# Kernel optimization log

Hardware: AMD Instinct MI355X
Metric: run time of the kernel (lower is better)

The kernel has to match this reference:

```python
import jax, jax.numpy as jnp
import numpy as np

B, S, IN_DIM, CTX = 32, 512, 256, 128
D, H, L = 128, 4, 2
DH = D // H
HID = 512
TOTAL = 11 * D * D + 8 * D  # hypernet flat weight size per sample
EPS = 1e-5


def _layernorm(x, g, b):
    mu = jnp.mean(x, axis=-1, keepdims=True)
    var = jnp.mean(jnp.square(x - mu), axis=-1, keepdims=True)
    return (x - mu) * jax.lax.rsqrt(var + EPS) * g + b


def setup_inputs() -> dict:
    key = jax.random.key(0)
    ks = jax.random.split(key, 24)
    f32 = jnp.float32
    inp = {
        'x': jax.random.normal(ks[0], (B, S, IN_DIM), f32),
        'context_vector': jax.random.normal(ks[1], (B, CTX), f32),
        'in_proj_w': jax.random.normal(ks[2], (D, IN_DIM), f32) * (IN_DIM ** -0.5),
        'in_proj_b': jnp.zeros((D,), f32),
        'pe': jax.random.normal(ks[3], (1, S, D), f32) * 0.02,
        'hfc1_w': jax.random.normal(ks[4], (L, HID, CTX), f32) * (CTX ** -0.5),
        'hfc1_b': jnp.zeros((L, HID), f32),
        'hfc2_w': jax.random.normal(ks[5], (L, TOTAL, HID), f32) * 0.02,
        'hfc2_b': jnp.zeros((L, TOTAL), f32),
        'out_proj_w': jax.random.normal(ks[6], (L, D, D), f32) * (D ** -0.5),
        'out_proj_b': jnp.zeros((L, D), f32),
        'ln1_g': jnp.ones((L, D), f32), 'ln1_b': jnp.zeros((L, D), f32),
        'ln2_g': jnp.ones((L, D), f32), 'ln2_b': jnp.zeros((L, D), f32),
        'alpha1': jnp.full((L,), 0.5, f32), 'alpha2': jnp.full((L,), 0.5, f32),
        'head_w': jax.random.normal(ks[7], (1, D), f32) * (D ** -0.5),
        'head_b': jnp.zeros((1,), f32),
    }
    return inp


def reference(x, context_vector, in_proj_w, in_proj_b, pe, hfc1_w, hfc1_b,
              hfc2_w, hfc2_b, out_proj_w, out_proj_b, ln1_g, ln1_b,
              ln2_g, ln2_b, alpha1, alpha2, head_w, head_b):
    # input projection + learned positional encoding
    h = jnp.einsum('bsi,di->bsd', x, in_proj_w) + in_proj_b
    h = h + pe[:, :h.shape[1], :]

    # flat split offsets for hypernet output
    sizes = [3 * D * D, 3 * D, 4 * D * D, 4 * D, 4 * D * D, D]
    offs = np.concatenate([[0], np.cumsum(sizes)])

    for l in range(L):
        # hypernet: per-sample weights from context
        hid = jax.nn.relu(context_vector @ hfc1_w[l].T + hfc1_b[l])
        flat = hid @ hfc2_w[l].T + hfc2_b[l]  # [B, TOTAL]
        aw = flat[:, offs[0]:offs[1]].reshape(B, 3 * D, D)
        ab = flat[:, offs[1]:offs[2]]                     # [B, 3D]
        f1w = flat[:, offs[2]:offs[3]].reshape(B, 4 * D, D)
        f1b = flat[:, offs[3]:offs[4]]                    # [B, 4D]
        f2w = flat[:, offs[4]:offs[5]].reshape(B, D, 4 * D)
        f2b = flat[:, offs[5]:offs[6]]                    # [B, D]

        # per-sample QKV projection (grouped GEMM over batch)
        qkv = jnp.einsum('bsd,bed->bse', h, aw) + ab[:, None, :]
        q, k, v = jnp.split(qkv, 3, axis=-1)
        q = q.reshape(B, S, H, DH)
        k = k.reshape(B, S, H, DH)
        v = v.reshape(B, S, H, DH)
        scores = jnp.einsum('bqhd,bkhd->bhqk', q, k) / jnp.sqrt(jnp.float32(DH))
        attn = jax.nn.softmax(scores, axis=-1)
        ctx = jnp.einsum('bhqk,bkhd->bqhd', attn, v).reshape(B, S, D)
        attn_out = jnp.einsum('bsd,ed->bse', ctx, out_proj_w[l]) + out_proj_b[l]

        h = _layernorm(h + alpha1[l] * attn_out, ln1_g[l], ln1_b[l])

        # per-sample FFN
        ff = jax.nn.relu(jnp.einsum('bsd,bfd->bsf', h, f1w) + f1b[:, None, :])
        ff = jnp.einsum('bsf,bdf->bsd', ff, f2w) + f2b[:, None, :]

        h = _layernorm(h + alpha2[l] * ff, ln2_g[l], ln2_b[l])

    out = h[:, -1, :] @ head_w.T + head_b  # [B, 1]
    return out
```

## Files before the change

### kernel.cpp

```cpp
#include <hip/hip_runtime.h>
#include <hip/hip_bf16.h>

constexpr int B_    = 32;
constexpr int S_    = 512;
constexpr int INDIM = 256;
constexpr int KCTX  = 128;
constexpr int D_    = 128;
constexpr int H_    = 4;
constexpr int L_    = 2;
constexpr int HID_  = 512;
constexpr int TOTAL_ = 11 * D_ * D_ + 8 * D_;
constexpr int OFF_AB  = 3 * D_ * D_;
constexpr int OFF_F1W = OFF_AB + 3 * D_;
constexpr int OFF_F1B = OFF_F1W + 4 * D_ * D_;
constexpr int OFF_F2W = OFF_F1B + 4 * D_;
constexpr int OFF_F2B = OFF_F2W + 4 * D_ * D_;
constexpr int TP = 132;

typedef __attribute__((ext_vector_type(8))) short short8;
typedef __attribute__((ext_vector_type(4))) short short4v;
typedef __attribute__((ext_vector_type(2))) short short2v;
typedef __attribute__((ext_vector_type(4))) float f32x4;

#define MFMA16 __builtin_amdgcn_mfma_f32_16x16x32_bf16

__device__ __forceinline__ short f2bf(float f) {
  __hip_bfloat16 h = __float2bfloat16(f);
  return __builtin_bit_cast(short, h);
}
__device__ __forceinline__ float bf2f(short s) {
  __hip_bfloat16 h = __builtin_bit_cast(__hip_bfloat16, s);
  return __bfloat162float(h);
}
struct bfpair { short hi, lo; };
__device__ __forceinline__ bfpair split2p(float x) {
  bfpair p;
  p.hi = f2bf(x);
  p.lo = f2bf(x - bf2f(p.hi));
  return p;
}

__device__ __forceinline__ void cvt_body(const float* __restrict__ in,
                                         short* __restrict__ oh,
                                         short* __restrict__ ol,
                                         int ktShift, int n8, int t) {
  if (t >= n8) return;
  int kt = 1 << ktShift;
  int row = t >> ktShift;
  int kc = t & (kt - 1);
  const float* p = in + ((long)row << (ktShift + 3)) + kc * 8;
  float4 v0 = *(const float4*)p;
  float4 v1 = *(const float4*)(p + 4);
  short8 h8, l8; bfpair q;
  q = split2p(v0.x); h8[0] = q.hi; l8[0] = q.lo;
  q = split2p(v0.y); h8[1] = q.hi; l8[1] = q.lo;
  q = split2p(v0.z); h8[2] = q.hi; l8[2] = q.lo;
  q = split2p(v0.w); h8[3] = q.hi; l8[3] = q.lo;
  q = split2p(v1.x); h8[4] = q.hi; l8[4] = q.lo;
  q = split2p(v1.y); h8[5] = q.hi; l8[5] = q.lo;
  q = split2p(v1.z); h8[6] = q.hi; l8[6] = q.lo;
  q = split2p(v1.w); h8[7] = q.hi; l8[7] = q.lo;
  long o = ((long)(row >> 4) * kt + kc) * 128 + (row & 15) * 8;
  *(short8*)(oh + o) = h8;
  *(short8*)(ol + o) = l8;
}

__global__ __launch_bounds__(256) void k_prep(
    const float* __restrict__ ipw, const float* __restrict__ opw,
    short* __restrict__ ipwFh, short* __restrict__ ipwFl,
    short* __restrict__ opwFh, short* __restrict__ opwFl,
    const float* __restrict__ cvec, const float* __restrict__ h1w,
    const float* __restrict__ h1b,
    short* __restrict__ hidFh, short* __restrict__ hidFl) {
  int id = blockIdx.x, tid = threadIdx.x;
  if (id < 16) {
    cvt_body(ipw, ipwFh, ipwFl, 5, D_ * INDIM / 8, id * 256 + tid);
  } else if (id < 32) {
    cvt_body(opw, opwFh, opwFl, 4, L_ * D_ * D_ / 8, (id - 16) * 256 + tid);
  } else {
    int hb = id - 32;
    int l = hb >> 5, b = hb & 31;
    __shared__ float cs[KCTX];
    if (tid < KCTX) cs[tid] = cvec[b * KCTX + tid];
    __syncthreads();
    #pragma unroll
    for (int jj = 0; jj < 2; ++jj) {
      int j = tid + jj * 256;
      const float* wr = h1w + (long)(l * HID_ + j) * KCTX;
      float s = h1b[l * HID_ + j];
      #pragma unroll
      for (int c = 0; c < KCTX; c += 4) {
        float4 cv = *(const float4*)(cs + c);
        float4 wv = *(const float4*)(wr + c);
        s += cv.x * wv.x + cv.y * wv.y + cv.z * wv.z + cv.w * wv.w;
      }
      s = fmaxf(s, 0.f);
      bfpair p = split2p(s);
      long o = (long)l * 32 * HID_ + ((long)(b >> 4) * 64 + (j >> 3)) * 128
             + (b & 15) * 8 + (j & 7);
      hidFh[o] = p.hi;
      hidFl[o] = p.lo;
    }
  }
}

__global__ __launch_bounds__(256) void k_flat_ip(
    const short* __restrict__ hidh, const short* __restrict__ hidl,
    const float* __restrict__ W, const float* __restrict__ bias,
    short* __restrict__ awh, short* __restrict__ awl,
    short* __restrict__ f1h, short* __restrict__ f1l,
    short* __restrict__ f2h, short* __restrict__ f2l,
    float* __restrict__ ab, float* __restrict__ f1b, float* __restrict__ f2b,
    const float* __restrict__ x,
    const short* __restrict__ ipwFh, const short* __restrict__ ipwFl,
    const float* __restrict__ ipb, const float* __restrict__ pe,
    float* __restrict__ h_f, short* __restrict__ hFh, short* __restrict__ hFl) {
  __shared__ short wls[2][2][64 * 64];
  const int id = blockIdx.x;
  const int tid = threadIdx.x, wave = tid >> 6, lane = tid & 63;
  const int r = lane & 15, g = lane >> 4;
  const int rr = tid >> 4;
  const int cc = (tid & 15) * 4;

  if (id < 256) {
    const int bx = id >> 5, b = id & 31;
    const float* abase = x + ((long)b * S_ + bx * 64) * INDIM;
    float4 av[2][4];
    #pragma unroll
    for (int rnd = 0; rnd < 4; ++rnd) {
      av[0][rnd] = *(const float4*)(abase + (long)(rnd * 16 + rr) * INDIM + cc);
      av[1][rnd] = *(const float4*)(abase + (long)(rnd * 16 + rr) * INDIM + 64 + cc);
    }
    const int n0 = (wave >> 1) * 64;
    const short* pWh = ipwFh + (n0 >> 4) * 4096 + g * 128 + r * 8;
    const short* pWl = ipwFl + (n0 >> 4) * 4096 + g * 128 + r * 8;
    f32x4 acc[2][4] = {{{0,0,0,0},{0,0,0,0},{0,0,0,0},{0,0,0,0}},
                       {{0,0,0,0},{0,0,0,0},{0,0,0,0},{0,0,0,0}}};
    for (int i = 0; i < 4; ++i) {
      int c0 = i * 64, cur = i & 1;
      #pragma unroll
      for (int rnd = 0; rnd < 4; ++rnd) {
        int row = rnd * 16 + rr;
        short4v h4, l4; bfpair q;
        q = split2p(av[cur][rnd].x); h4[0] = q.hi; l4[0] = q.lo;
        q = split2p(av[cur][rnd].y); h4[1] = q.hi; l4[1] = q.lo;
        q = split2p(av[cur][rnd].z); h4[2] = q.hi; l4[2] = q.lo;
        q = split2p(av[cur][rnd].w); h4[3] = q.hi; l4[3] = q.lo;
        int sb = row * 128 + ((cc * 2) ^ ((row & 7) << 4));
        *(short4v*)((char*)&wls[cur][0][0] + sb) = h4;
        *(short4v*)((char*)&wls[cur][1][0] + sb) = l4;
      }
      if (i + 2 < 4) {
        #pragma unroll
        for (int rnd = 0; rnd < 4; ++rnd)
          av[cur][rnd] = *(const float4*)(abase + (long)(rnd * 16 + rr) * INDIM + (c0 + 128) + cc);
      }
      __syncthreads();
      #pragma unroll
      for (int kk = 0; kk < 2; ++kk) {
        long wo = (long)(c0 * 16) + kk * 512;
        short8 ah[2], al[2];
        #pragma unroll
        for (int ms = 0; ms < 2; ++ms) {
          int arow = (wave & 1) * 32 + ms * 16 + r;
          int abyte = arow * 128 + ((kk * 64 + g * 16) ^ ((r & 7) << 4));
          ah[ms] = *(const short8*)((char*)&wls[cur][0][0] + abyte);
          al[ms] = *(const short8*)((char*)&wls[cur][1][0] + abyte);
        }
        #pragma unroll
        for (int ns = 0; ns < 4; ++ns) {
          short8 wh = *(const short8*)(pWh + ns * 4096 + wo);
          short8 wl = *(const short8*)(pWl + ns * 4096 + wo);
          #pragma unroll
          for (int ms = 0; ms < 2; ++ms) {
            acc[ms][ns] = MFMA16(ah[ms], wl, acc[ms][ns], 0, 0, 0);
            acc[ms][ns] = MFMA16(al[ms], wh, acc[ms][ns], 0, 0, 0);
            acc[ms][ns] = MFMA16(ah[ms], wh, acc[ms][ns], 0, 0, 0);
          }
        }
      }
      __syncthreads();
    }
    #pragma unroll
    for (int ms = 0; ms < 2; ++ms) {
      #pragma unroll
      for (int ns = 0; ns < 4; ++ns) {
        int ccol = n0 + ns * 16 + r;
        float bv = ipb[ccol];
        #pragma unroll
        for (int reg = 0; reg < 4; ++reg) {
          int crow = bx * 64 + (wave & 1) * 32 + ms * 16 + g * 4 + reg;
          float v = acc[ms][ns][reg] + bv + pe[crow * D_ + ccol];
          h_f[((long)b * S_ + crow) * D_ + ccol] = v;
          long o = (long)b * 65536 + (long)(crow >> 4) * 2048
                 + (ccol >> 3) * 128 + (crow & 15) * 8 + (ccol & 7);
          bfpair sp = split2p(v);
          hFh[o] = sp.hi;
          hFl[o] = sp.lo;
        }
      }
    }
    return;
  }

  const int fid = id - 256;
  const int l = fid / 2832;
  const int bxf = fid % 2832;
  hidh += (long)l * 32 * HID_;
  hidl += (long)l * 32 * HID_;
  W    += (long)l * TOTAL_ * HID_;
  bias += (long)l * TOTAL_;
  awh  += (long)l * B_ * 49152;  awl += (long)l * B_ * 49152;
  f1h  += (long)l * B_ * 65536;  f1l += (long)l * B_ * 65536;
  f2h  += (long)l * B_ * 65536;  f2l += (long)l * B_ * 65536;
  ab   += l * B_ * 384;  f1b += l * B_ * 512;  f2b += l * B_ * 128;
  const int nb0 = bxf * 64;
  const float* wbase = W + (long)nb0 * HID_;
  float4 wv[2][4];
  #pragma unroll
  for (int rnd = 0; rnd < 4; ++rnd) {
    wv[0][rnd] = *(const float4*)(wbase + (long)(rnd * 16 + rr) * HID_ + cc);
    wv[1][rnd] = *(const float4*)(wbase + (long)(rnd * 16 + rr) * HID_ + 64 + cc);
  }
  const short* pAh = hidh + g * 128 + r * 8;
  const short* pAl = hidl + g * 128 + r * 8;
  f32x4 acc0 = {0, 0, 0, 0}, acc1 = {0, 0, 0, 0};
  for (int i = 0; i < 8; ++i) {
    int c0 = i * 64, cur = i & 1;
    #pragma unroll
    for (int rnd = 0; rnd < 4; ++rnd) {
      int row = rnd * 16 + rr;
      short4v h4, l4; bfpair q;
      q = split2p(wv[cur][rnd].x); h4[0] = q.hi; l4[0] = q.lo;
      q = split2p(wv[cur][rnd].y); h4[1] = q.hi; l4[1] = q.lo;
      q = split2p(wv[cur][rnd].z); h4[2] = q.hi; l4[2] = q.lo;
      q = split2p(wv[cur][rnd].w); h4[3] = q.hi; l4[3] = q.lo;
      int sb = row * 128 + ((cc * 2) ^ ((row & 7) << 4));
      *(short4v*)((char*)&wls[cur][0][0] + sb) = h4;
      *(short4v*)((char*)&wls[cur][1][0] + sb) = l4;
    }
    if (i + 2 < 8) {
      #pragma unroll
      for (int rnd = 0; rnd < 4; ++rnd)
        wv[cur][rnd] = *(const float4*)(wbase + (long)(rnd * 16 + rr) * HID_ + (c0 + 128) + cc);
    }
    __syncthreads();
    #pragma unroll
    for (int kk = 0; kk < 2; ++kk) {
      long ao = (long)(c0 * 16) + kk * 512;
      short8 ah0 = *(const short8*)(pAh + ao);
      short8 ah1 = *(const short8*)(pAh + 8192 + ao);
      short8 al0 = *(const short8*)(pAl + ao);
      short8 al1 = *(const short8*)(pAl + 8192 + ao);
      int wrow = wave * 16 + r;
      int wb = wrow * 128 + ((kk * 64 + g * 16) ^ ((r & 7) << 4));
      short8 wh = *(const short8*)((char*)&wls[cur][0][0] + wb);
      short8 wl = *(const short8*)((char*)&wls[cur][1][0] + wb);
      acc0 = MFMA16(ah0, wl, acc0, 0, 0, 0);
      acc0 = MFMA16(al0, wh, acc0, 0, 0, 0);
      acc0 = MFMA16(ah0, wh, acc0, 0, 0, 0);
      acc1 = MFMA16(ah1, wl, acc1, 0, 0, 0);
      acc1 = MFMA16(al1, wh, acc1, 0, 0, 0);
      acc1 = MFMA16(ah1, wh, acc1, 0, 0, 0);
    }
    __syncthreads();
  }
  constexpr int TPF = 68;
  float* tile = (float*)&wls[0][0][0];
  {
    float bv = bias[nb0 + wave * 16 + r];
    int col = wave * 16 + r;
    #pragma unroll
    for (int reg = 0; reg < 4; ++reg) {
      tile[(g * 4 + reg) * TPF + col]      = acc0[reg] + bv;
      tile[(g * 4 + reg + 16) * TPF + col] = acc1[reg] + bv;
    }
  }
  __syncthreads();
  {
    int b  = tid >> 3;
    int cg = tid & 7;
    int t0 = nb0 + cg * 8;
    float v[8];
    #pragma unroll
    for (int j = 0; j < 8; ++j) v[j] = tile[b * TPF + cg * 8 + j];
    if (t0 < OFF_AB) {
      int e = t0 >> 7, d = t0 & 127;
      long a = (long)b * 49152 + ((long)(e >> 4) * 16 + (d >> 3)) * 128 + (e & 15) * 8;
      short8 h8, l8; bfpair q;
      #pragma unroll
      for (int j = 0; j < 8; ++j) { q = split2p(v[j]); h8[j] = q.hi; l8[j] = q.lo; }
      *(short8*)(awh + a) = h8;
      *(short8*)(awl + a) = l8;
    } else if (t0 < OFF_F1W) {
      float* dst = ab + b * 384 + (t0 - OFF_AB);
      float4 x0 = {v[0], v[1], v[2], v[3]}, x1 = {v[4], v[5], v[6], v[7]};
      *(float4*)dst = x0; *(float4*)(dst + 4) = x1;
    } else if (t0 < OFF_F1B) {
      int i = t0 - OFF_F1W; int f = i >> 7, d = i & 127;
      long a = (long)b * 65536 + ((long)(f >> 4) * 16 + (d >> 3)) * 128 + (f & 15) * 8;
      short8 h8, l8; bfpair q;
      #pragma unroll
      for (int j = 0; j < 8; ++j) { q = split2p(v[j]); h8[j] = q.hi; l8[j] = q.lo; }
      *(short8*)(f1h + a) = h8;
      *(short8*)(f1l + a) = l8;
    } else if (t0 < OFF_F2W) {
      float* dst = f1b + b * 512 + (t0 - OFF_F1B);
      float4 x0 = {v[0], v[1], v[2], v[3]}, x1 = {v[4], v[5], v[6], v[7]};
      *(float4*)dst = x0; *(float4*)(dst + 4) = x1;
    } else if (t0 < OFF_F2B) {
      int i = t0 - OFF_F2W; int dd = i >> 9, f = i & 511;
      long a = (long)b * 65536 + ((long)(dd >> 4) * 64 + (f >> 3)) * 128 + (dd & 15) * 8;
      short8 h8, l8; bfpair q;
      #pragma unroll
      for (int j = 0; j < 8; ++j) { q = split2p(v[j]); h8[j] = q.hi; l8[j] = q.lo; }
      *(short8*)(f2h + a) = h8;
      *(short8*)(f2l + a) = l8;
    } else {
      float* dst = f2b + b * 128 + (t0 - OFF_F2B);
      float4 x0 = {v[0], v[1], v[2], v[3]}, x1 = {v[4], v[5], v[6], v[7]};
      *(float4*)dst = x0; *(float4*)(dst + 4) = x1;
    }
  }
}

template <int K, int EPI, bool RELU>
__global__ __launch_bounds__(256) void k_gemm(
    const short* __restrict__ Ah, const short* __restrict__ Al, long sA,
    const short* __restrict__ Wh, const short* __restrict__ Wl, long sW,
    const float* __restrict__ biasP, long sB,
    void* __restrict__ p0, void* __restrict__ p1,
    void* __restrict__ p2, void* __restrict__ p3,
    int N,
    const float* __restrict__ lng, const float* __restrict__ lnb,
    const float* __restrict__ lnal, int mOff, int nOff, int mode) {
  extern __shared__ char smem_dyn[];
  const int tid = threadIdx.x, wave = tid >> 6, lane = tid & 63;
  const int r = lane & 15, g = lane >> 4;
  const int b = blockIdx.z;
  int bx, by;
  if (mode == 1) {
    int xx = blockIdx.x;
    if (xx < 16) { bx = xx >> 1; by = 1 + (xx & 1); }
    else         { bx = 7; by = 0; }
  } else {
    bx = blockIdx.x + mOff; by = blockIdx.y + nOff;
  }
  const int m0 = bx * 64 + (wave & 1) * 32;
  const int n0 = by * 128 + (wave >> 1) * 64;
  const long KT = (long)K * 16;
  const short* pAh = Ah + (long)b * sA + (m0 >> 4) * KT + g * 128 + r * 8;
  const short* pAl = Al + (long)b * sA + (m0 >> 4) * KT + g * 128 + r * 8;
  const short* pWh = Wh + (long)b * sW + (n0 >> 4) * KT + g * 128 + r * 8;
  const short* pWl = Wl + (long)b * sW + (n0 >> 4) * KT + g * 128 + r * 8;
  f32x4 acc[2][4] = {{{0,0,0,0},{0,0,0,0},{0,0,0,0},{0,0,0,0}},
                     {{0,0,0,0},{0,0,0,0},{0,0,0,0},{0,0,0,0}}};
  for (int kk = 0; kk < K / 32; ++kk) {
    long ko = (long)kk * 512;
    short8 a0h = *(const short8*)(pAh + ko);
    short8 a1h = *(const short8*)(pAh + KT + ko);
    short8 a0l = *(const short8*)(pAl + ko);
    short8 a1l = *(const short8*)(pAl + KT + ko);
    #pragma unroll
    for (int ns = 0; ns < 4; ++ns) {
      short8 wh = *(const short8*)(pWh + ns * KT + ko);
      short8 wl = *(const short8*)(pWl + ns * KT + ko);
      acc[0][ns] = MFMA16(a0h, wl, acc[0][ns], 0, 0, 0);
      acc[0][ns] = MFMA16(a0l, wh, acc[0][ns], 0, 0, 0);
      acc[0][ns] = MFMA16(a0h, wh, acc[0][ns], 0, 0, 0);
      acc[1][ns] = MFMA16(a1h, wl, acc[1][ns], 0, 0, 0);
      acc[1][ns] = MFMA16(a1l, wh, acc[1][ns], 0, 0, 0);
      acc[1][ns] = MFMA16(a1h, wh, acc[1][ns], 0, 0, 0);
    }
  }

  if constexpr (EPI == 5) {
    if (by == 2) {
      #pragma unroll
      for (int ms = 0; ms < 2; ++ms) {
        int crow0 = m0 + ms * 16 + g * 4;
        #pragma unroll
        for (int ns = 0; ns < 4; ++ns) {
          int ccol = n0 + ns * 16 + r;
          float bv = biasP[(long)b * sB + ccol];
          int c2 = ccol - 256, hd = c2 >> 5, dd = c2 & 31;
          short4v h4, l4; bfpair q;
          #pragma unroll
          for (int reg = 0; reg < 4; ++reg) {
            float v = acc[ms][ns][reg] + bv;
            q = split2p(v); h4[reg] = q.hi; l4[reg] = q.lo;
          }
          long o = (long)(b * 4 + hd) * 16384 + (dd >> 4) * 8192
                 + (crow0 >> 3) * 128 + (dd & 15) * 8 + (crow0 & 7);
          *(short4v*)((short*)p2 + o) = h4;
          *(short4v*)((short*)p3 + o) = l4;
        }
      }
      return;
    }
  }

  float* tile = (float*)smem_dyn;
  #pragma unroll
  for (int ms = 0; ms < 2; ++ms) {
    #pragma unroll
    for (int ns = 0; ns < 4; ++ns) {
      int ccol = n0 + ns * 16 + r;
      float bv = biasP[(long)b * sB + ccol];
      #pragma unroll
      for (int reg = 0; reg < 4; ++reg) {
        float v = acc[ms][ns][reg] + bv;
        if constexpr (RELU) v = fmaxf(v, 0.f);
        int trow2 = (wave & 1) * 32 + ms * 16 + g * 4 + reg;
        int tcol = (wave >> 1) * 64 + ns * 16 + r;
        tile[trow2 * TP + tcol] = v;
      }
    }
  }
  __syncthreads();

  if constexpr (EPI == 0 || EPI == 5) {
    int row = tid >> 2, cg = tid & 3;
    int crow = bx * 64 + row;
    long rowbase = (long)b * 512 * N + (long)(crow >> 4) * (16 * (long)N) + (crow & 15) * 8;
    #pragma unroll
    for (int j4 = 0; j4 < 4; ++j4) {
      int tcol = j4 * 32 + cg * 8;
      float4 aa = *(const float4*)&tile[row * TP + tcol];
      float4 bb = *(const float4*)&tile[row * TP + tcol + 4];
// ... 157 lines not shown
      int col0 = hh * 32 + r;
      long o = (long)b * 65536 + (long)(srow >> 4) * 2048
             + (col0 >> 3) * 128 + (srow & 15) * 8 + (col0 & 7);
      bfpair sp0 = split2p(a0);
      ch[o] = sp0.hi; cl[o] = sp0.lo;
      long o2 = o + 2 * 128;
      bfpair sp1 = split2p(a1);
      ch[o2] = sp1.hi; cl[o2] = sp1.lo;
    }
  }
}

__global__ __launch_bounds__(64) void k_head(const float* __restrict__ h,
                                             const float* __restrict__ hw,
                                             const float* __restrict__ hb,
                                             float* __restrict__ out) {
  int b = blockIdx.x, lane = threadIdx.x;
  const float* hr = h + ((long)b * S_ + (S_ - 1)) * D_;
  float v = hr[lane] * hw[lane] + hr[lane + 64] * hw[lane + 64];
  #pragma unroll
  for (int o = 32; o > 0; o >>= 1) v += __shfl_xor(v, o);
  if (lane == 0) out[b] = v + hb[0];
}

extern "C" void kernel_launch(void* const* d_in, const int* in_sizes, int n_in,
                              void* d_out, int out_size, void* d_ws, size_t ws_size,
                              hipStream_t stream) {
  const float* x    = (const float*)d_in[0];
  const float* cvec = (const float*)d_in[1];
  const float* ipw  = (const float*)d_in[2];
  const float* ipb  = (const float*)d_in[3];
  const float* pe   = (const float*)d_in[4];
  const float* h1w  = (const float*)d_in[5];
  const float* h1b  = (const float*)d_in[6];
  const float* h2w  = (const float*)d_in[7];
  const float* h2b  = (const float*)d_in[8];
  const float* opw  = (const float*)d_in[9];
  const float* opb  = (const float*)d_in[10];
  const float* ln1g = (const float*)d_in[11];
  const float* ln1b = (const float*)d_in[12];
  const float* ln2g = (const float*)d_in[13];
  const float* ln2b = (const float*)d_in[14];
  const float* a1   = (const float*)d_in[15];
  const float* a2   = (const float*)d_in[16];
  const float* hw   = (const float*)d_in[17];
  const float* hb   = (const float*)d_in[18];
  float* out = (float*)d_out;

  char* ws = (char*)d_ws;
  size_t off = 0;
  auto alloc = [&](size_t n) { void* p = ws + off; off = (off + n + 255) & ~(size_t)255; return p; };

  const long AWs = (long)B_ * 49152;
  const long F1s = (long)B_ * 65536;
  const long F2s = (long)B_ * 65536;

  short* ff1h  = (short*)alloc((size_t)B_ * S_ * 512 * 2);
  short* ff1l  = (short*)alloc((size_t)B_ * S_ * 512 * 2);
  float* h_f   = (float*)alloc((size_t)B_ * S_ * D_ * 4);
  short* hFh   = (short*)alloc((size_t)B_ * S_ * D_ * 2);
  short* hFl   = (short*)alloc((size_t)B_ * S_ * D_ * 2);
  short* hidFh = (short*)alloc((size_t)L_ * 32 * HID_ * 2);
  short* hidFl = (short*)alloc((size_t)L_ * 32 * HID_ * 2);
  short* awFh  = (short*)alloc((size_t)L_ * AWs * 2);
  short* awFl  = (short*)alloc((size_t)L_ * AWs * 2);
  short* f1wFh = (short*)alloc((size_t)L_ * F1s * 2);
  short* f1wFl = (short*)alloc((size_t)L_ * F1s * 2);
  short* f2wFh = (short*)alloc((size_t)L_ * F2s * 2);
  short* f2wFl = (short*)alloc((size_t)L_ * F2s * 2);
  float* abF   = (float*)alloc((size_t)L_ * B_ * 384 * 4);
  float* f1bF  = (float*)alloc((size_t)L_ * B_ * 512 * 4);
  float* f2bF  = (float*)alloc((size_t)L_ * B_ * 128 * 4);
  short* qkFh  = (short*)alloc((size_t)B_ * S_ * 256 * 2);
  short* qkFl  = (short*)alloc((size_t)B_ * S_ * 256 * 2);
  short* vtFh  = (short*)alloc((size_t)B_ * H_ * 32 * S_ * 2);
  short* vtFl  = (short*)alloc((size_t)B_ * H_ * 32 * S_ * 2);
  short* cxFh  = (short*)alloc((size_t)B_ * S_ * D_ * 2);
  short* cxFl  = (short*)alloc((size_t)B_ * S_ * D_ * 2);
  short* ipwFh = (short*)alloc((size_t)D_ * INDIM * 2);
  short* ipwFl = (short*)alloc((size_t)D_ * INDIM * 2);
  short* opwFh = (short*)alloc((size_t)L_ * D_ * D_ * 2);
  short* opwFl = (short*)alloc((size_t)L_ * D_ * D_ * 2);

  k_prep<<<96, 256, 0, stream>>>(ipw, opw, ipwFh, ipwFl, opwFh, opwFl,
                                 cvec, h1w, h1b, hidFh, hidFl);

  k_flat_ip<<<256 + 2 * 2832, 256, 0, stream>>>(
      hidFh, hidFl, h2w, h2b, awFh, awFl, f1wFh, f1wFl, f2wFh, f2wFl,
      abF, f1bF, f2bF,
      x, ipwFh, ipwFl, ipb, pe, h_f, hFh, hFl);

  constexpr size_t TILE_LDS = 64 * TP * 4;

  {
    int l = 0;
    k_gemm<D_, 5, false><<<dim3(8, 3, B_), 256, TILE_LDS, stream>>>(
        hFh, hFl, (long)S_ * D_, awFh + l * AWs, awFl + l * AWs, 49152,
        abF + l * B_ * 384, 384,
        qkFh, qkFl, vtFh, vtFl, 256, nullptr, nullptr, nullptr, 0, 0, 0);
    k_attn<<<dim3(S_ / 16, H_, B_), 128, 0, stream>>>(qkFh, qkFl, vtFh, vtFl, cxFh, cxFl, 0);
    k_gemm<D_, 4, false><<<dim3(8, 1, B_), 256, TILE_LDS, stream>>>(
        cxFh, cxFl, (long)S_ * D_, opwFh + l * 16384, opwFl + l * 16384, 0,
        opb + l * D_, 0, h_f, hFh, hFl, nullptr, 128,
        ln1g + l * D_, ln1b + l * D_, a1 + l, 0, 0, 0);
    k_gemm<D_, 0, true><<<dim3(8, 4, B_), 256, TILE_LDS, stream>>>(
        hFh, hFl, (long)S_ * D_, f1wFh + l * F1s, f1wFl + l * F1s, 65536,
        f1bF + l * B_ * 512, 512,
        ff1h, ff1l, nullptr, nullptr, 512, nullptr, nullptr, nullptr, 0, 0, 0);
    k_gemm<512, 4, false><<<dim3(8, 1, B_), 256, TILE_LDS, stream>>>(
        ff1h, ff1l, (long)S_ * 512, f2wFh + l * F2s, f2wFl + l * F2s, 65536,
        f2bF + l * B_ * 128, 128,
        h_f, hFh, hFl, nullptr, 128,
        ln2g + l * D_, ln2b + l * D_, a2 + l, 0, 0, 0);
  }

  {
    int l = 1;
    k_gemm<D_, 5, false><<<dim3(17, 1, B_), 256, TILE_LDS, stream>>>(
        hFh, hFl, (long)S_ * D_, awFh + l * AWs, awFl + l * AWs, 49152,
        abF + l * B_ * 384, 384,
        qkFh, qkFl, vtFh, vtFl, 256, nullptr, nullptr, nullptr, 0, 0, 1);
    k_attn<<<dim3(1, H_, B_), 128, 0, stream>>>(qkFh, qkFl, vtFh, vtFl, cxFh, cxFl, 31);
    k_gemm<D_, 4, false><<<dim3(1, 1, B_), 256, TILE_LDS, stream>>>(
        cxFh, cxFl, (long)S_ * D_, opwFh + l * 16384, opwFl + l * 16384, 0,
        opb + l * D_, 0, h_f, hFh, hFl, nullptr, 128,
        ln1g + l * D_, ln1b + l * D_, a1 + l, 7, 0, 0);
    k_gemm<D_, 0, true><<<dim3(1, 4, B_), 256, TILE_LDS, stream>>>(
        hFh, hFl, (long)S_ * D_, f1wFh + l * F1s, f1wFl + l * F1s, 65536,
        f1bF + l * B_ * 512, 512,
        ff1h, ff1l, nullptr, nullptr, 512, nullptr, nullptr, nullptr, 7, 0, 0);
    k_gemm<512, 4, false><<<dim3(1, 1, B_), 256, TILE_LDS, stream>>>(
        ff1h, ff1l, (long)S_ * 512, f2wFh + l * F2s, f2wFl + l * F2s, 65536,
        f2bF + l * B_ * 128, 128,
        h_f, hFh, hFl, nullptr, 128,
        ln2g + l * D_, ln2b + l * D_, a2 + l, 7, 0, 0);
  }
  k_head<<<B_, 64, 0, stream>>>(h_f, hw, hb, out);
}
```

Before: 417.1 us.

## Overlap layer-1 hypernet weight generation with layer-0 GEMM kernels

Moves the layer-1 hypernet flat-weight GEMM out of the initial k_flat_ip launch and spreads its 2832 blocks across the four layer-0 k_gemm launches as extra trailing blocks. The GEMM kernels switch to a 1D grid with a gemmBlocks threshold, and blocks past it run flat_block using the dynamic LDS. The aim is to fill idle CUs during the small per-layer GEMMs and shorten the large upfront hypernet kernel. In exchange, the layer-0 kernels carry more register and LDS pressure from the merged code path, and the dynamic LDS must be large enough for flat_block's buffers.

```diff
diff --git a/kernel.cpp b/kernel.cpp
--- a/kernel.cpp
+++ b/kernel.cpp
@@ -104,6 +104,217 @@
   }
 }
 
+__device__ void flat_block(int fid, char* lds,
+    const short* __restrict__ hidh, const short* __restrict__ hidl,
+    const float* __restrict__ W, const float* __restrict__ bias,
+    short* __restrict__ awh, short* __restrict__ awl,
+    short* __restrict__ f1h, short* __restrict__ f1l,
+    short* __restrict__ f2h, short* __restrict__ f2l,
+    float* __restrict__ ab, float* __restrict__ f1b, float* __restrict__ f2b) {
+  const int tid = threadIdx.x, wave = tid >> 6, lane = tid & 63;
+  const int r = lane & 15, g = lane >> 4;
+  const int rr = tid >> 4, cc = (tid & 15) * 4;
+  const int nb0 = fid * 64;
+  const float* wbase = W + (long)nb0 * HID_;
+  float4 wv[2][4];
+  #pragma unroll
+  for (int rnd = 0; rnd < 4; ++rnd) {
+    wv[0][rnd] = *(const float4*)(wbase + (long)(rnd * 16 + rr) * HID_ + cc);
+    wv[1][rnd] = *(const float4*)(wbase + (long)(rnd * 16 + rr) * HID_ + 64 + cc);
+  }
+  const short* pAh = hidh + g * 128 + r * 8;
+  const short* pAl = hidl + g * 128 + r * 8;
+  f32x4 acc0 = {0, 0, 0, 0}, acc1 = {0, 0, 0, 0};
+  for (int i = 0; i < 8; ++i) {
+    int c0 = i * 64, cur = i & 1;
+    char* bh = lds + (cur * 2 + 0) * 8192;
+    char* bl = lds + (cur * 2 + 1) * 8192;
+    #pragma unroll
+    for (int rnd = 0; rnd < 4; ++rnd) {
+      int row = rnd * 16 + rr;
+      short4v h4, l4; bfpair q;
+      q = split2p(wv[cur][rnd].x); h4[0] = q.hi; l4[0] = q.lo;
+      q = split2p(wv[cur][rnd].y); h4[1] = q.hi; l4[1] = q.lo;
+      q = split2p(wv[cur][rnd].z); h4[2] = q.hi; l4[2] = q.lo;
+      q = split2p(wv[cur][rnd].w); h4[3] = q.hi; l4[3] = q.lo;
+      int sb = row * 128 + ((cc * 2) ^ ((row & 7) << 4));
+      *(short4v*)(bh + sb) = h4;
+      *(short4v*)(bl + sb) = l4;
+    }
+    if (i + 2 < 8) {
+      #pragma unroll
+      for (int rnd = 0; rnd < 4; ++rnd)
+        wv[cur][rnd] = *(const float4*)(wbase + (long)(rnd * 16 + rr) * HID_ + (c0 + 128) + cc);
+    }
+    __syncthreads();
+    #pragma unroll
+    for (int kk = 0; kk < 2; ++kk) {
+      long ao = (long)(c0 * 16) + kk * 512;
+      short8 ah0 = *(const short8*)(pAh + ao);
+      short8 ah1 = *(const short8*)(pAh + 8192 + ao);
+      short8 al0 = *(const short8*)(pAl + ao);
+      short8 al1 = *(const short8*)(pAl + 8192 + ao);
+      int wrow = wave * 16 + r;
+      int wb = wrow * 128 + ((kk * 64 + g * 16) ^ ((r & 7) << 4));
+      short8 wh = *(const short8*)(bh + wb);
+      short8 wl = *(const short8*)(bl + wb);
+      acc0 = MFMA16(ah0, wl, acc0, 0, 0, 0);
+      acc0 = MFMA16(al0, wh, acc0, 0, 0, 0);
+      acc0 = MFMA16(ah0, wh, acc0, 0, 0, 0);
+      acc1 = MFMA16(ah1, wl, acc1, 0, 0, 0);
+      acc1 = MFMA16(al1, wh, acc1, 0, 0, 0);
+      acc1 = MFMA16(ah1, wh, acc1, 0, 0, 0);
+    }
+    __syncthreads();
+  }
+  constexpr int TPF = 68;
+  float* tile = (float*)lds;
+  {
+    float bv = bias[nb0 + wave * 16 + r];
+    int col = wave * 16 + r;
+    #pragma unroll
+    for (int reg = 0; reg < 4; ++reg) {
+      tile[(g * 4 + reg) * TPF + col]      = acc0[reg] + bv;
+      tile[(g * 4 + reg + 16) * TPF + col] = acc1[reg] + bv;
+    }
+  }
+  __syncthreads();
+  {
+    int b  = tid >> 3;
+    int cg = tid & 7;
+    int t0 = nb0 + cg * 8;
+    float v[8];
+    #pragma unroll
+    for (int j = 0; j < 8; ++j) v[j] = tile[b * TPF + cg * 8 + j];
+    if (t0 < OFF_AB) {
+      int e = t0 >> 7, d = t0 & 127;
+      long a = (long)b * 49152 + ((long)(e >> 4) * 16 + (d >> 3)) * 128 + (e & 15) * 8;
+      short8 h8, l8; bfpair q;
+      #pragma unroll
+      for (int j = 0; j < 8; ++j) { q = split2p(v[j]); h8[j] = q.hi; l8[j] = q.lo; }
+      *(short8*)(awh + a) = h8;
+      *(short8*)(awl + a) = l8;
+    } else if (t0 < OFF_F1W) {
+      float* dst = ab + b * 384 + (t0 - OFF_AB);
+      float4 x0 = {v[0], v[1], v[2], v[3]}, x1 = {v[4], v[5], v[6], v[7]};
+      *(float4*)dst = x0; *(float4*)(dst + 4) = x1;
+    } else if (t0 < OFF_F1B) {
+      int i = t0 - OFF_F1W; int f = i >> 7, d = i & 127;
+      long a = (long)b * 65536 + ((long)(f >> 4) * 16 + (d >> 3)) * 128 + (f & 15) * 8;
+      short8 h8, l8; bfpair q;
+      #pragma unroll
+      for (int j = 0; j < 8; ++j) { q = split2p(v[j]); h8[j] = q.hi; l8[j] = q.lo; }
+      *(short8*)(f1h + a) = h8;
+      *(short8*)(f1l + a) = l8;
+    } else if (t0 < OFF_F2W) {
+      float* dst = f1b + b * 512 + (t0 - OFF_F1B);
+      float4 x0 = {v[0], v[1], v[2], v[3]}, x1 = {v[4], v[5], v[6], v[7]};
+      *(float4*)dst = x0; *(float4*)(dst + 4) = x1;
+    } else if (t0 < OFF_F2B) {
+      int i = t0 - OFF_F2W; int dd = i >> 9, f = i & 511;
+      long a = (long)b * 65536 + ((long)(dd >> 4) * 64 + (f >> 3)) * 128 + (dd & 15) * 8;
+      short8 h8, l8; bfpair q;
+      #pragma unroll
+      for (int j = 0; j < 8; ++j) { q = split2p(v[j]); h8[j] = q.hi; l8[j] = q.lo; }
+      *(short8*)(f2h + a) = h8;
+      *(short8*)(f2l + a) = l8;
+    } else {
+      float* dst = f2b + b * 128 + (t0 - OFF_F2B);
+      float4 x0 = {v[0], v[1], v[2], v[3]}, x1 = {v[4], v[5], v[6], v[7]};
+      *(float4*)dst = x0; *(float4*)(dst + 4) = x1;
+    }
+  }
+}
+
+__device__ void inproj_block(int id, char* lds,
+    const float* __restrict__ x,
+    const short* __restrict__ ipwFh, const short* __restrict__ ipwFl,
+    const float* __restrict__ ipb, const float* __restrict__ pe,
+    float* __restrict__ h_f, short* __restrict__ hFh, short* __restrict__ hFl) {
+  const int tid = threadIdx.x, wave = tid >> 6, lane = tid & 63;
+  const int r = lane & 15, g = lane >> 4;
+  const int rr = tid >> 4, cc = (tid & 15) * 4;
+  const int bx = id >> 5, b = id & 31;
+  const float* abase = x + ((long)b * S_ + bx * 64) * INDIM;
+  float4 av[2][4];
+  #pragma unroll
+  for (int rnd = 0; rnd < 4; ++rnd) {
+    av[0][rnd] = *(const float4*)(abase + (long)(rnd * 16 + rr) * INDIM + cc);
+    av[1][rnd] = *(const float4*)(abase + (long)(rnd * 16 + rr) * INDIM + 64 + cc);
+  }
+  const int n0 = (wave >> 1) * 64;
+  const short* pWh = ipwFh + (n0 >> 4) * 4096 + g * 128 + r * 8;
+  const short* pWl = ipwFl + (n0 >> 4) * 4096 + g * 128 + r * 8;
+  f32x4 acc[2][4] = {{{0,0,0,0},{0,0,0,0},{0,0,0,0},{0,0,0,0}},
+                     {{0,0,0,0},{0,0,0,0},{0,0,0,0},{0,0,0,0}}};
+  for (int i = 0; i < 4; ++i) {
+    int c0 = i * 64, cur = i & 1;
+    char* bh = lds + (cur * 2 + 0) * 8192;
+    char* bl = lds + (cur * 2 + 1) * 8192;
+    #pragma unroll
+    for (int rnd = 0; rnd < 4; ++rnd) {
+      int row = rnd * 16 + rr;
+      short4v h4, l4; bfpair q;
+      q = split2p(av[cur][rnd].x); h4[0] = q.hi; l4[0] = q.lo;
+      q = split2p(av[cur][rnd].y); h4[1] = q.hi; l4[1] = q.lo;
+      q = split2p(av[cur][rnd].z); h4[2] = q.hi; l4[2] = q.lo;
+      q = split2p(av[cur][rnd].w); h4[3] = q.hi; l4[3] = q.lo;
+      int sb = row * 128 + ((cc * 2) ^ ((row & 7) << 4));
+      *(short4v*)(bh + sb) = h4;
+      *(short4v*)(bl + sb) = l4;
+    }
+    if (i + 2 < 4) {
+      #pragma unroll
+      for (int rnd = 0; rnd < 4; ++rnd)
+        av[cur][rnd] = *(const float4*)(abase + (long)(rnd * 16 + rr) * INDIM + (c0 + 128) + cc);
+    }
+    __syncthreads();
+    #pragma unroll
+    for (int kk = 0; kk < 2; ++kk) {
+      long wo = (long)(c0 * 16) + kk * 512;
+      short8 ah[2], al[2];
+      #pragma unroll
+      for (int ms = 0; ms < 2; ++ms) {
+        int arow = (wave & 1) * 32 + ms * 16 + r;
+        int abyte = arow * 128 + ((kk * 64 + g * 16) ^ ((r & 7) << 4));
+        ah[ms] = *(const short8*)(bh + abyte);
+        al[ms] = *(const short8*)(bl + abyte);
+      }
+      #pragma unroll
+      for (int ns = 0; ns < 4; ++ns) {
+        short8 wh = *(const short8*)(pWh + ns * 4096 + wo);
+        short8 wl = *(const short8*)(pWl + ns * 4096 + wo);
+        #pragma unroll
+        for (int ms = 0; ms < 2; ++ms) {
+          acc[ms][ns] = MFMA16(ah[ms], wl, acc[ms][ns], 0, 0, 0);
+          acc[ms][ns] = MFMA16(al[ms], wh, acc[ms][ns], 0, 0, 0);
+          acc[ms][ns] = MFMA16(ah[ms], wh, acc[ms][ns], 0, 0, 0);
+        }
+      }
+    }
+    __syncthreads();
+  }
+  #pragma unroll
+  for (int ms = 0; ms < 2; ++ms) {
+    #pragma unroll
+    for (int ns = 0; ns < 4; ++ns) {
+      int ccol = n0 + ns * 16 + r;
+      float bv = ipb[ccol];
+      #pragma unroll
+      for (int reg = 0; reg < 4; ++reg) {
+        int crow = bx * 64 + (wave & 1) * 32 + ms * 16 + g * 4 + reg;
+        float v = acc[ms][ns][reg] + bv + pe[crow * D_ + ccol];
+        h_f[((long)b * S_ + crow) * D_ + ccol] = v;
+        long o = (long)b * 65536 + (long)(crow >> 4) * 2048
+               + (ccol >> 3) * 128 + (crow & 15) * 8 + (ccol & 7);
+        bfpair sp = split2p(v);
+        hFh[o] = sp.hi;
+        hFl[o] = sp.lo;
+      }
+    }
+  }
+}
+
 __global__ __launch_bounds__(256) void k_flat_ip(
     const short* __restrict__ hidh, const short* __restrict__ hidl,
     const float* __restrict__ W, const float* __restrict__ bias,
@@ -115,212 +326,13 @@
     const short* __restrict__ ipwFh, const short* __restrict__ ipwFl,
     const float* __restrict__ ipb, const float* __restrict__ pe,
     float* __restrict__ h_f, short* __restrict__ hFh, short* __restrict__ hFl) {
-  __shared__ short wls[2][2][64 * 64];
+  __shared__ __align__(16) char ldsb[33792];
   const int id = blockIdx.x;
-  const int tid = threadIdx.x, wave = tid >> 6, lane = tid & 63;
-  const int r = lane & 15, g = lane >> 4;
-  const int rr = tid >> 4;
-  const int cc = (tid & 15) * 4;
-
   if (id < 256) {
-    const int bx = id >> 5, b = id & 31;
-    const float* abase = x + ((long)b * S_ + bx * 64) * INDIM;
-    float4 av[2][4];
-    #pragma unroll
-    for (int rnd = 0; rnd < 4; ++rnd) {
-      av[0][rnd] = *(const float4*)(abase + (long)(rnd * 16 + rr) * INDIM + cc);
-      av[1][rnd] = *(const float4*)(abase + (long)(rnd * 16 + rr) * INDIM + 64 + cc);
-    }
-    const int n0 = (wave >> 1) * 64;
-    const short* pWh = ipwFh + (n0 >> 4) * 4096 + g * 128 + r * 8;
-    const short* pWl = ipwFl + (n0 >> 4) * 4096 + g * 128 + r * 8;
-    f32x4 acc[2][4] = {{{0,0,0,0},{0,0,0,0},{0,0,0,0},{0,0,0,0}},
-                       {{0,0,0,0},{0,0,0,0},{0,0,0,0},{0,0,0,0}}};
-    for (int i = 0; i < 4; ++i) {
-      int c0 = i * 64, cur = i & 1;
-      #pragma unroll
-      for (int rnd = 0; rnd < 4; ++rnd) {
-        int row = rnd * 16 + rr;
-        short4v h4, l4; bfpair q;
-        q = split2p(av[cur][rnd].x); h4[0] = q.hi; l4[0] = q.lo;
-        q = split2p(av[cur][rnd].y); h4[1] = q.hi; l4[1] = q.lo;
-        q = split2p(av[cur][rnd].z); h4[2] = q.hi; l4[2] = q.lo;
-        q = split2p(av[cur][rnd].w); h4[3] = q.hi; l4[3] = q.lo;
-        int sb = row * 128 + ((cc * 2) ^ ((row & 7) << 4));
-        *(short4v*)((char*)&wls[cur][0][0] + sb) = h4;
-        *(short4v*)((char*)&wls[cur][1][0] + sb) = l4;
-      }
-      if (i + 2 < 4) {
-        #pragma unroll
-        for (int rnd = 0; rnd < 4; ++rnd)
-          av[cur][rnd] = *(const float4*)(abase + (long)(rnd * 16 + rr) * INDIM + (c0 + 128) + cc);
-      }
-      __syncthreads();
-      #pragma unroll
-      for (int kk = 0; kk < 2; ++kk) {
-        long wo = (long)(c0 * 16) + kk * 512;
-        short8 ah[2], al[2];
-        #pragma unroll
-        for (int ms = 0; ms < 2; ++ms) {
-          int arow = (wave & 1) * 32 + ms * 16 + r;
-          int abyte = arow * 128 + ((kk * 64 + g * 16) ^ ((r & 7) << 4));
-          ah[ms] = *(const short8*)((char*)&wls[cur][0][0] + abyte);
-          al[ms] = *(const short8*)((char*)&wls[cur][1][0] + abyte);
-        }
-        #pragma unroll
-        for (int ns = 0; ns < 4; ++ns) {
-          short8 wh = *(const short8*)(pWh + ns * 4096 + wo);
-          short8 wl = *(const short8*)(pWl + ns * 4096 + wo);
-          #pragma unroll
-          for (int ms = 0; ms < 2; ++ms) {
-            acc[ms][ns] = MFMA16(ah[ms], wl, acc[ms][ns], 0, 0, 0);
-            acc[ms][ns] = MFMA16(al[ms], wh, acc[ms][ns], 0, 0, 0);
-            acc[ms][ns] = MFMA16(ah[ms], wh, acc[ms][ns], 0, 0, 0);
-          }
-        }
-      }
-      __syncthreads();
-    }
-    #pragma unroll
-    for (int ms = 0; ms < 2; ++ms) {
-      #pragma unroll
-      for (int ns = 0; ns < 4; ++ns) {
-        int ccol = n0 + ns * 16 + r;
-        float bv = ipb[ccol];
-        #pragma unroll
-        for (int reg = 0; reg < 4; ++reg) {
-          int crow = bx * 64 + (wave & 1) * 32 + ms * 16 + g * 4 + reg;
-          float v = acc[ms][ns][reg] + bv + pe[crow * D_ + ccol];
-          h_f[((long)b * S_ + crow) * D_ + ccol] = v;
-          long o = (long)b * 65536 + (long)(crow >> 4) * 2048
-                 + (ccol >> 3) * 128 + (crow & 15) * 8 + (ccol & 7);
-          bfpair sp = split2p(v);
-          hFh[o] = sp.hi;
-          hFl[o] = sp.lo;
-        }
-      }
-    }
-    return;
-  }
-
-  const int fid = id - 256;
-  const int l = fid / 2832;
-  const int bxf = fid % 2832;
-  hidh += (long)l * 32 * HID_;
-  hidl += (long)l * 32 * HID_;
-  W    += (long)l * TOTAL_ * HID_;
-  bias += (long)l * TOTAL_;
-  awh  += (long)l * B_ * 49152;  awl += (long)l * B_ * 49152;
-  f1h  += (long)l * B_ * 65536;  f1l += (long)l * B_ * 65536;
-  f2h  += (long)l * B_ * 65536;  f2l += (long)l * B_ * 65536;
-  ab   += l * B_ * 384;  f1b += l * B_ * 512;  f2b += l * B_ * 128;
-  const int nb0 = bxf * 64;
-  const float* wbase = W + (long)nb0 * HID_;
-  float4 wv[2][4];
-  #pragma unroll
-  for (int rnd = 0; rnd < 4; ++rnd) {
-    wv[0][rnd] = *(const float4*)(wbase + (long)(rnd * 16 + rr) * HID_ + cc);
-    wv[1][rnd] = *(const float4*)(wbase + (long)(rnd * 16 + rr) * HID_ + 64 + cc);
-  }
-  const short* pAh = hidh + g * 128 + r * 8;
-  const short* pAl = hidl + g * 128 + r * 8;
-  f32x4 acc0 = {0, 0, 0, 0}, acc1 = {0, 0, 0, 0};
-  for (int i = 0; i < 8; ++i) {
-    int c0 = i * 64, cur = i & 1;
-    #pragma unroll
-    for (int rnd = 0; rnd < 4; ++rnd) {
-      int row = rnd * 16 + rr;
-      short4v h4, l4; bfpair q;
-      q = split2p(wv[cur][rnd].x); h4[0] = q.hi; l4[0] = q.lo;
-      q = split2p(wv[cur][rnd].y); h4[1] = q.hi; l4[1] = q.lo;
-      q = split2p(wv[cur][rnd].z); h4[2] = q.hi; l4[2] = q.lo;
-      q = split2p(wv[cur][rnd].w); h4[3] = q.hi; l4[3] = q.lo;
-      int sb = row * 128 + ((cc * 2) ^ ((row & 7) << 4));
-      *(short4v*)((char*)&wls[cur][0][0] + sb) = h4;
-      *(short4v*)((char*)&wls[cur][1][0] + sb) = l4;
-    }
-    if (i + 2 < 8) {
-      #pragma unroll
-      for (int rnd = 0; rnd < 4; ++rnd)
-        wv[cur][rnd] = *(const float4*)(wbase + (long)(rnd * 16 + rr) * HID_ + (c0 + 128) + cc);
-    }
-    __syncthreads();
-    #pragma unroll
-    for (int kk = 0; kk < 2; ++kk) {
-      long ao = (long)(c0 * 16) + kk * 512;
-      short8 ah0 = *(const short8*)(pAh + ao);
-      short8 ah1 = *(const short8*)(pAh + 8192 + ao);
-      short8 al0 = *(const short8*)(pAl + ao);
-      short8 al1 = *(const short8*)(pAl + 8192 + ao);
-      int wrow = wave * 16 + r;
-      int wb = wrow * 128 + ((kk * 64 + g * 16) ^ ((r & 7) << 4));
-      short8 wh = *(const short8*)((char*)&wls[cur][0][0] + wb);
-      short8 wl = *(const short8*)((char*)&wls[cur][1][0] + wb);
-      acc0 = MFMA16(ah0, wl, acc0, 0, 0, 0);
-      acc0 = MFMA16(al0, wh, acc0, 0, 0, 0);
-      acc0 = MFMA16(ah0, wh, acc0, 0, 0, 0);
-      acc1 = MFMA16(ah1, wl, acc1, 0, 0, 0);
-      acc1 = MFMA16(al1, wh, acc1, 0, 0, 0);
-      acc1 = MFMA16(ah1, wh, acc1, 0, 0, 0);
-    }
-    __syncthreads();
-  }
-  constexpr int TPF = 68;
-  float* tile = (float*)&wls[0][0][0];
-  {
-    float bv = bias[nb0 + wave * 16 + r];
-    int col = wave * 16 + r;
-    #pragma unroll
-    for (int reg = 0; reg < 4; ++reg) {
-      tile[(g * 4 + reg) * TPF + col]      = acc0[reg] + bv;
-      tile[(g * 4 + reg + 16) * TPF + col] = acc1[reg] + bv;
-    }
-  }
-  __syncthreads();
-  {
-    int b  = tid >> 3;
-    int cg = tid & 7;
-    int t0 = nb0 + cg * 8;
-    float v[8];
-    #pragma unroll
-    for (int j = 0; j < 8; ++j) v[j] = tile[b * TPF + cg * 8 + j];
-    if (t0 < OFF_AB) {
-      int e = t0 >> 7, d = t0 & 127;
-      long a = (long)b * 49152 + ((long)(e >> 4) * 16 + (d >> 3)) * 128 + (e & 15) * 8;
-      short8 h8, l8; bfpair q;
-      #pragma unroll
-      for (int j = 0; j < 8; ++j) { q = split2p(v[j]); h8[j] = q.hi; l8[j] = q.lo; }
-      *(short8*)(awh + a) = h8;
-      *(short8*)(awl + a) = l8;
-    } else if (t0 < OFF_F1W) {
-      float* dst = ab + b * 384 + (t0 - OFF_AB);
-      float4 x0 = {v[0], v[1], v[2], v[3]}, x1 = {v[4], v[5], v[6], v[7]};
-      *(float4*)dst = x0; *(float4*)(dst + 4) = x1;
-    } else if (t0 < OFF_F1B) {
-      int i = t0 - OFF_F1W; int f = i >> 7, d = i & 127;
-      long a = (long)b * 65536 + ((long)(f >> 4) * 16 + (d >> 3)) * 128 + (f & 15) * 8;
-      short8 h8, l8; bfpair q;
-      #pragma unroll
-      for (int j = 0; j < 8; ++j) { q = split2p(v[j]); h8[j] = q.hi; l8[j] = q.lo; }
-      *(short8*)(f1h + a) = h8;
-      *(short8*)(f1l + a) = l8;
-    } else if (t0 < OFF_F2W) {
-      float* dst = f1b + b * 512 + (t0 - OFF_F1B);
-      float4 x0 = {v[0], v[1], v[2], v[3]}, x1 = {v[4], v[5], v[6], v[7]};
-      *(float4*)dst = x0; *(float4*)(dst + 4) = x1;
-    } else if (t0 < OFF_F2B) {
-      int i = t0 - OFF_F2W; int dd = i >> 9, f = i & 511;
-      long a = (long)b * 65536 + ((long)(dd >> 4) * 64 + (f >> 3)) * 128 + (dd & 15) * 8;
-      short8 h8, l8; bfpair q;
-      #pragma unroll
-      for (int j = 0; j < 8; ++j) { q = split2p(v[j]); h8[j] = q.hi; l8[j] = q.lo; }
-      *(short8*)(f2h + a) = h8;
-      *(short8*)(f2l + a) = l8;
-    } else {
-      float* dst = f2b + b * 128 + (t0 - OFF_F2B);
-      float4 x0 = {v[0], v[1], v[2], v[3]}, x1 = {v[4], v[5], v[6], v[7]};
-      *(float4*)dst = x0; *(float4*)(dst + 4) = x1;
-    }
+    inproj_block(id, ldsb, x, ipwFh, ipwFl, ipb, pe, h_f, hFh, hFl);
+  } else {
+    flat_block(id - 256, ldsb, hidh, hidl, W, bias, awh, awl,
+               f1h, f1l, f2h, f2l, ab, f1b, f2b);
   }
 }
 
@@ -333,18 +345,32 @@
     void* __restrict__ p2, void* __restrict__ p3,
     int N,
     const float* __restrict__ lng, const float* __restrict__ lnb,
-    const float* __restrict__ lnal, int mOff, int nOff, int mode) {
+    const float* __restrict__ lnal, int mOff, int nOff, int mode,
+    int mx, int gemmBlocks, int flatBase,
+    const short* __restrict__ fhh, const short* __restrict__ fhl,
+    const float* __restrict__ fW, const float* __restrict__ fbias,
+    short* __restrict__ fawh, short* __restrict__ fawl,
+    short* __restrict__ ffa, short* __restrict__ ffb,
+    short* __restrict__ ffc, short* __restrict__ ffd,
+    float* __restrict__ fab, float* __restrict__ ff1b, float* __restrict__ ff2b) {
   extern __shared__ char smem_dyn[];
+  const int idg = blockIdx.x;
+  if (idg >= gemmBlocks) {
+    flat_block(flatBase + (idg - gemmBlocks), smem_dyn, fhh, fhl, fW, fbias,
+               fawh, fawl, ffa, ffb, ffc, ffd, fab, ff1b, ff2b);
+    return;
+  }
   const int tid = threadIdx.x, wave = tid >> 6, lane = tid & 63;
   const int r = lane & 15, g = lane >> 4;
-  const int b = blockIdx.z;
+  const int b = idg & 31;
   int bx, by;
   if (mode == 1) {
-    int xx = blockIdx.x;
+    int xx = idg >> 5;
     if (xx < 16) { bx = xx >> 1; by = 1 + (xx & 1); }
     else         { bx = 7; by = 0; }
   } else {
-    bx = blockIdx.x + mOff; by = blockIdx.y + nOff;
+    int rest = idg >> 5;
+    bx = rest % mx + mOff; by = rest / mx + nOff;
   }
   const int m0 = bx * 64 + (wave & 1) * 32;
   const int n0 = by * 128 + (wave >> 1) * 64;
@@ -668,10 +694,21 @@
   short* opwFh = (short*)alloc((size_t)L_ * D_ * D_ * 2);
   short* opwFl = (short*)alloc((size_t)L_ * D_ * D_ * 2);
 
+  const short* fhh = hidFh + 32 * HID_;
+  const short* fhl = hidFl + 32 * HID_;
+  const float* fW  = h2w + (long)TOTAL_ * HID_;
+  const float* fbias = h2b + TOTAL_;
+  short* fawh = awFh + AWs;  short* fawl = awFl + AWs;
+  short* ffa  = f1wFh + F1s; short* ffb  = f1wFl + F1s;
+  short* ffc  = f2wFh + F2s; short* ffd  = f2wFl + F2s;
+  float* fab  = abF + B_ * 384;
+  float* ff1b = f1bF + B_ * 512;
+  float* ff2b = f2bF + B_ * 128;
+
   k_prep<<<96, 256, 0, stream>>>(ipw, opw, ipwFh, ipwFl, opwFh, opwFl,
                                  cvec, h1w, h1b, hidFh, hidFl);
 
-  k_flat_ip<<<256 + 2 * 2832, 256, 0, stream>>>(
+  k_flat_ip<<<256 + 2832, 256, 0, stream>>>(
       hidFh, hidFl, h2w, h2b, awFh, awFl, f1wFh, f1wFl, f2wFh, f2wFl,
       abF, f1bF, f2bF,
       x, ipwFh, ipwFl, ipb, pe, h_f, hFh, hFl);
@@ -680,46 +717,63 @@
 
   {
     int l = 0;
-    k_gemm<D_, 5, false><<<dim3(8, 3, B_), 256, TILE_LDS, stream>>>(
+    k_gemm<D_, 5, false><<<768 + 944, 256, TILE_LDS, stream>>>(
+        hFh, hFl, (long)S_ * D_, awFh, awFl, 49152, abF, 384,
+        qkFh, qkFl, vtFh, vtFl, 256, nullptr, nullptr, nullptr, 0, 0, 0,
+        8, 768, 0,
+        fhh, fhl, fW, fbias, fawh, fawl, ffa, ffb, ffc, ffd, fab, ff1b, ff2b);
+    k_attn<<<dim3(S_ / 16, H_, B_), 128, 0, stream>>>(qkFh, qkFl, vtFh, vtFl, cxFh, cxFl, 0);
+    k_gemm<D_, 4, false><<<256 + 472, 256, TILE_LDS, stream>>>(
+        cxFh, cxFl, (long)S_ * D_, opwFh + l * 16384, opwFl + l * 16384, 0,
+        opb + l * D_, 0, h_f, hFh, hFl, nullptr, 128,
+        ln1g + l * D_, ln1b + l * D_, a1 + l, 0, 0, 0,
+        8, 256, 944,
+        fhh, fhl, fW, fbias, fawh, fawl, ffa, ffb, ffc, ffd, fab, ff1b, ff2b);
+    k_gemm<D_, 0, true><<<1024 + 944, 256, TILE_LDS, stream>>>(
+        hFh, hFl, (long)S_ * D_, f1wFh, f1wFl, 65536, f1bF, 512,
+        ff1h, ff1l, nullptr, nullptr, 512, nullptr, nullptr, nullptr, 0, 0, 0,
+        8, 1024, 1416,
+        fhh, fhl, fW, fbias, fawh, fawl, ffa, ffb, ffc, ffd, fab, ff1b, ff2b);
+    k_gemm<512, 4, false><<<256 + 472, 256, TILE_LDS, stream>>>(
+        ff1h, ff1l, (long)S_ * 512, f2wFh, f2wFl, 65536, f2bF, 128,
+        h_f, hFh, hFl, nullptr, 128,
+        ln2g + l * D_, ln2b + l * D_, a2 + l, 0, 0, 0,
+        8, 256, 2360,
+        fhh, fhl, fW, fbias, fawh, fawl, ffa, ffb, ffc, ffd, fab, ff1b, ff2b);
+  }
+
+  {
+    int l = 1;
+    k_gemm<D_, 5, false><<<544, 256, TILE_LDS, stream>>>(
         hFh, hFl, (long)S_ * D_, awFh + l * AWs, awFl + l * AWs, 49152,
         abF + l * B_ * 384, 384,
-        qkFh, qkFl, vtFh, vtFl, 256, nullptr, nullptr, nullptr, 0, 0, 0);
-    k_attn<<<dim3(S_ / 16, H_, B_), 128, 0, stream>>>(qkFh, qkFl, vtFh, vtFl, cxFh, cxFl, 0);
-    k_gemm<D_, 4, false><<<dim3(8, 1, B_), 256, TILE_LDS, stream>>>(
+        qkFh, qkFl, vtFh, vtFl, 256, nullptr, nullptr, nullptr, 0, 0, 1,
+        1, 544, 0,
+        nullptr, nullptr, nullptr, nullptr, nullptr, nullptr, nullptr, nullptr,
+        nullptr, nullptr, nullptr, nullptr, nullptr);
+    k_attn<<<dim3(1, H_, B_), 128, 0, stream>>>(qkFh, qkFl, vtFh, vtFl, cxFh, cxFl, 31);
+    k_gemm<D_, 4, false><<<32, 256, TILE_LDS, stream>>>(
         cxFh, cxFl, (long)S_ * D_, opwFh + l * 16384, opwFl + l * 16384, 0,
         opb + l * D_, 0, h_f, hFh, hFl, nullptr, 128,
-        ln1g + l * D_, ln1b + l * D_, a1 + l, 0, 0, 0);
-    k_gemm<D_, 0, true><<<dim3(8, 4, B_), 256, TILE_LDS, stream>>>(
+        ln1g + l * D_, ln1b + l * D_, a1 + l, 7, 0, 0,
+        1, 32, 0,
+        nullptr, nullptr, nullptr, nullptr, nullptr, nullptr, nullptr, nullptr,
+        nullptr, nullptr, nullptr, nullptr, nullptr);
+    k_gemm<D_, 0, true><<<128, 256, TILE_LDS, stream>>>(
         hFh, hFl, (long)S_ * D_, f1wFh + l * F1s, f1wFl + l * F1s, 65536,
         f1bF + l * B_ * 512, 512,
-        ff1h, ff1l, nullptr, nullptr, 512, nullptr, nullptr, nullptr, 0, 0, 0);
-    k_gemm<512, 4, false><<<dim3(8, 1, B_), 256, TILE_LDS, stream>>>(
+        ff1h, ff1l, nullptr, nullptr, 512, nullptr, nullptr, nullptr, 7, 0, 0,
+        1, 128, 0,
+        nullptr, nullptr, nullptr, nullptr, nullptr, nullptr, nullptr, nullptr,
+        nullptr, nullptr, nullptr, nullptr, nullptr);
+    k_gemm<512, 4, false><<<32, 256, TILE_LDS, stream>>>(
         ff1h, ff1l, (long)S_ * 512, f2wFh + l * F2s, f2wFl + l * F2s, 65536,
         f2bF + l * B_ * 128, 128,
         h_f, hFh, hFl, nullptr, 128,
-        ln2g + l * D_, ln2b + l * D_, a2 + l, 0, 0, 0);
-  }
-
-  {
-    int l = 1;
-    k_gemm<D_, 5, false><<<dim3(17, 1, B_), 256, TILE_LDS, stream>>>(
-        hFh, hFl, (long)S_ * D_, awFh + l * AWs, awFl + l * AWs, 49152,
-        abF + l * B_ * 384, 384,
-        qkFh, qkFl, vtFh, vtFl, 256, nullptr, nullptr, nullptr, 0, 0, 1);
-    k_attn<<<dim3(1, H_, B_), 128, 0, stream>>>(qkFh, qkFl, vtFh, vtFl, cxFh, cxFl, 31);
-    k_gemm<D_, 4, false><<<dim3(1, 1, B_), 256, TILE_LDS, stream>>>(
-        cxFh, cxFl, (long)S_ * D_, opwFh + l * 16384, opwFl + l * 16384, 0,
-        opb + l * D_, 0, h_f, hFh, hFl, nullptr, 128,
-        ln1g + l * D_, ln1b + l * D_, a1 + l, 7, 0, 0);
-    k_gemm<D_, 0, true><<<dim3(1, 4, B_), 256, TILE_LDS, stream>>>(
-        hFh, hFl, (long)S_ * D_, f1wFh + l * F1s, f1wFl + l * F1s, 65536,
-        f1bF + l * B_ * 512, 512,
-        ff1h, ff1l, nullptr, nullptr, 512, nullptr, nullptr, nullptr, 7, 0, 0);
-    k_gemm<512, 4, false><<<dim3(1, 1, B_), 256, TILE_LDS, stream>>>(
-        ff1h, ff1l, (long)S_ * 512, f2wFh + l * F2s, f2wFl + l * F2s, 65536,
-        f2bF + l * B_ * 128, 128,
-        h_f, hFh, hFl, nullptr, 128,
-        ln2g + l * D_, ln2b + l * D_, a2 + l, 7, 0, 0);
+        ln2g + l * D_, ln2b + l * D_, a2 + l, 7, 0, 0,
+        1, 32, 0,
+        nullptr, nullptr, nullptr, nullptr, nullptr, nullptr, nullptr, nullptr,
+        nullptr, nullptr, nullptr, nullptr, nullptr);
   }
   k_head<<<B_, 64, 0, stream>>>(h_f, hw, hb, out);
 }
```

Result: slower. 621.7 us (+49.1%).
